# Kernel tuning notes

Hardware: AMD Instinct MI355X
Metric: run time of the kernel (lower is better)

Reference implementation:

```python
import jax, jax.numpy as jnp
import numpy as np

NUM_HEADS = 16
ROPE_BASE = 10000.0


def _rope_cos_sin(seq_len, head_dim, dtype):
    inv_freq = 1.0 / (ROPE_BASE ** (jnp.arange(0, head_dim, 2, dtype=jnp.float32) / head_dim))
    t = jnp.arange(seq_len, dtype=jnp.float32)
    freqs = jnp.einsum('i,j->ij', t, inv_freq)          # [S, hd/2]
    emb = jnp.concatenate([freqs, freqs], axis=-1)      # [S, hd]
    return jnp.cos(emb).astype(dtype), jnp.sin(emb).astype(dtype)


def _rotate_half(x):
    x1, x2 = jnp.split(x, 2, axis=-1)
    return jnp.concatenate([-x2, x1], axis=-1)


def setup_inputs() -> dict:
    key = jax.random.key(0)
    k1, k2, k3 = jax.random.split(key, 3)
    B, S, D = 2, 2048, 2048
    x = jax.random.normal(k1, (B, S, D), dtype=jnp.float32)
    w_qkv = jax.random.normal(k2, (D, 3 * D), dtype=jnp.float32) * (D ** -0.5)
    w_out = jax.random.normal(k3, (D, D), dtype=jnp.float32) * (D ** -0.5)
    return {"x": x, "w_qkv": w_qkv, "w_out": w_out}


def reference(x, w_qkv, w_out):
    B, S, D = x.shape
    H = NUM_HEADS
    hd = D // H
    scale = hd ** -0.5

    qkv = jnp.einsum('bsd,de->bse', x, w_qkv)            # [B,S,3D]
    q, k, v = jnp.split(qkv, 3, axis=-1)
    # -> [B,H,S,hd]
    q = q.reshape(B, S, H, hd).transpose(0, 2, 1, 3)
    k = k.reshape(B, S, H, hd).transpose(0, 2, 1, 3)
    v = v.reshape(B, S, H, hd).transpose(0, 2, 1, 3)

    cos, sin = _rope_cos_sin(S, hd, x.dtype)             # [S,hd]
    cos = cos[None, None]                                # [1,1,S,hd]
    sin = sin[None, None]
    q = q * cos + _rotate_half(q) * sin
    k = k * cos + _rotate_half(k) * sin

    scores = jnp.einsum('bhqd,bhkd->bhqk', q, k) * scale  # [B,H,S,S]
    attn = jax.nn.softmax(scores, axis=-1)                # non-causal: no mask
    out = jnp.einsum('bhqk,bhkd->bhqd', attn, v)          # [B,H,S,hd]
    out = out.transpose(0, 2, 1, 3).reshape(B, S, D)
    out = jnp.einsum('bsd,de->bse', out, w_out)
    return out
```

## Files before the change

kernel.cpp:

```cpp
#include <hip/hip_runtime.h>
#include <hip/hip_bf16.h>

typedef __hip_bfloat16 bf16_t;
typedef __bf16 bf16x8 __attribute__((ext_vector_type(8)));
typedef float floatx4 __attribute__((ext_vector_type(4)));

#define DEVINL __device__ __forceinline__

DEVINL floatx4 mfma16(bf16x8 a, bf16x8 b, floatx4 c) {
  return __builtin_amdgcn_mfma_f32_16x16x32_bf16(a, b, c, 0, 0, 0);
}

DEVINL void gload_lds16(const bf16_t* gp, bf16_t* lp) {
  __builtin_amdgcn_global_load_lds(
      (const __attribute__((address_space(1))) unsigned int*)gp,
      (__attribute__((address_space(3))) unsigned int*)lp, 16, 0, 0);
}

template <class CT> DEVINL CT cvtC(float f);
template <> DEVINL bf16_t cvtC<bf16_t>(float f) { return __float2bfloat16(f); }
template <> DEVINL float cvtC<float>(float f) { return f; }

DEVINL unsigned int pack_bf2(float a, float b) {
  union { bf16_t h; unsigned short s; } ua, ub;
  ua.h = __float2bfloat16(a);
  ub.h = __float2bfloat16(b);
  return (unsigned int)ua.s | ((unsigned int)ub.s << 16);
}

__global__ void convert_f32_bf16(const float* __restrict__ in,
                                 bf16_t* __restrict__ out) {
  size_t i = ((size_t)blockIdx.x * 256 + threadIdx.x) * 8;
  floatx4 a = *(const floatx4*)(in + i);
  floatx4 b = *(const floatx4*)(in + i + 4);
  bf16x8 r;
#pragma unroll
  for (int j = 0; j < 4; j++) r[j] = (__bf16)a[j];
#pragma unroll
  for (int j = 0; j < 4; j++) r[4 + j] = (__bf16)b[j];
  *(bf16x8*)(out + i) = r;
}

template <bool SPLITV, class CT>
__global__ __launch_bounds__(512, 2) void gemm128(
    const bf16_t* __restrict__ A, const bf16_t* __restrict__ BT,
    CT* __restrict__ C, bf16_t* __restrict__ VTout, int M, int N, int CN,
    int K) {
  extern __shared__ __align__(16) char smem[];
  bf16_t* a_lds = (bf16_t*)smem;
  bf16_t* b_lds = a_lds + 24576;

  const int tid = threadIdx.x;
  const int w = tid >> 6;
  const int lane = tid & 63;
  const int quad = lane >> 4;
  const int l16 = lane & 15;
  const int wm = w >> 2, wn = w & 3;

  const int cpx = (int)gridDim.x >> 3;
  const int wgid = ((int)blockIdx.x & 7) * cpx + ((int)blockIdx.x >> 3);
  const int nym = M >> 7;
  const int row0 = (wgid % nym) * 128;
  const int col0 = (wgid / nym) * 256;

  floatx4 acc[4][4] = {};
  bf16x8 af[4][2], bfr[2][2];

  const int nfE = (w >> 1) * 4 + (w & 1);
  const bf16_t* agA = A + (size_t)(row0 + w * 16 + l16) * K + quad * 8;
  const bf16_t* agB = BT + (size_t)(col0 + nfE * 16 + l16) * K + quad * 8;

#define STG_A(sb, tt)                                                      \
  {                                                                        \
    _Pragma("unroll") for (int kc = 0; kc < 2; kc++)                       \
        gload_lds16(agA + (tt) * 64 + kc * 32,                             \
                    a_lds + (sb) * 8192 + w * 1024 + kc * 512);            \
  }
#define STG_BE(sb, tt)                                                     \
  {                                                                        \
    _Pragma("unroll") for (int kc = 0; kc < 2; kc++)                       \
        gload_lds16(agB + (tt) * 64 + kc * 32,                             \
                    b_lds + (sb) * 16384 + nfE * 1024 + kc * 512);         \
  }
#define STG_BO(sb, tt)                                                     \
  {                                                                        \
    _Pragma("unroll") for (int kc = 0; kc < 2; kc++)                       \
        gload_lds16(agB + (size_t)32 * K + (tt) * 64 + kc * 32,            \
                    b_lds + (sb) * 16384 + (nfE + 2) * 1024 + kc * 512);   \
  }
#define LDA(cb)                                                            \
  {                                                                        \
    _Pragma("unroll") for (int m = 0; m < 4; m++)                          \
        _Pragma("unroll") for (int kc = 0; kc < 2; kc++)                   \
            af[m][kc] = *(const bf16x8*)(a_lds + (cb) * 8192 +             \
                                         (wm * 4 + m) * 1024 + kc * 512 +  \
                                         lane * 8);                        \
  }
#define LDB(cb, h)                                                         \
  {                                                                        \
    _Pragma("unroll") for (int jj = 0; jj < 2; jj++)                       \
        _Pragma("unroll") for (int kc = 0; kc < 2; kc++)                   \
            bfr[jj][kc] = *(const bf16x8*)(b_lds + (cb) * 16384 +          \
                                           (wn * 4 + 2 * (h) + jj) * 1024 + \
                                           kc * 512 + lane * 8);           \
  }
#define MM(h)                                                              \
  {                                                                        \
    __builtin_amdgcn_s_setprio(1);                                         \
    _Pragma("unroll") for (int kc = 0; kc < 2; kc++)                       \
        _Pragma("unroll") for (int m = 0; m < 4; m++)                      \
            _Pragma("unroll") for (int jj = 0; jj < 2; jj++)               \
                acc[m][2 * (h) + jj] = mfma16(af[m][kc], bfr[jj][kc],      \
                                              acc[m][2 * (h) + jj]);       \
    __builtin_amdgcn_s_setprio(0);                                         \
  }
#define BAR() __builtin_amdgcn_s_barrier();
#define VM(n) asm volatile("s_waitcnt vmcnt(" #n ")" ::: "memory");
#define LGK() asm volatile("s_waitcnt lgkmcnt(0)" ::: "memory");

#define TILE(tt, cb, sb, DOSTG, V0m, V1m)                  \
  {                                                        \
     LDA(cb); LDB(cb, 0);                            \
    if (DOSTG) { STG_A(sb, (tt) + 2); STG_BE(sb, (tt) + 2); } \
    V0m BAR(); LGK(); MM(0); BAR();                        \
     LDB(cb, 1);                                     \
    if (DOSTG) { STG_BO(sb, (tt) + 2); }                   \
    V1m BAR(); LGK(); MM(1); BAR();                        \
  }

  STG_A(0, 0); STG_BE(0, 0); STG_BO(0, 0);
  STG_A(1, 1); STG_BE(1, 1); STG_BO(1, 1);
  VM(8);
  __builtin_amdgcn_s_barrier();

  const int nt = K >> 6;
  for (int t = 0; t < nt - 2; t += 3) {
    TILE(t, 0, 2, 1, VM(10);, VM(8);)
    TILE(t + 1, 1, 0, 1, VM(10);, VM(8);)
    TILE(t + 2, 2, 1, 1, VM(10);, VM(8);)
  }
  TILE(nt - 2, 0, 0, 0, VM(6);, VM(2);)
  TILE(nt - 1, 1, 0, 0, VM(0);, )

#undef TILE
#undef LGK
#undef VM
#undef BAR
#undef MM
#undef LDB
#undef LDA
#undef STG_BO
#undef STG_BE
#undef STG_A

  if (!SPLITV || col0 < 4096) {
#pragma unroll
    for (int m = 0; m < 4; m++)
#pragma unroll
      for (int n = 0; n < 4; n++)
#pragma unroll
        for (int r = 0; r < 4; r++) {
          int row = row0 + wm * 64 + m * 16 + quad * 4 + r;
          int col = col0 + wn * 64 + n * 16 + l16;
          C[(size_t)row * CN + col] = cvtC<CT>(acc[m][n][r]);
        }
  } else {
    const int b = row0 >> 11;
    const int s0 = row0 & 2047;
    const int h = ((col0 - 4096) >> 7) + (wn >> 1);
    bf16_t* vt = VTout + (size_t)(b * 16 + h) * 128 * 2048;
    struct __align__(8) bf4 { bf16_t v[4]; };
#pragma unroll
    for (int m = 0; m < 4; m++)
#pragma unroll
      for (int n = 0; n < 4; n++) {
        int d = (wn & 1) * 64 + n * 16 + l16;
        int s = s0 + wm * 64 + m * 16 + quad * 4;
        bf4 o;
#pragma unroll
        for (int r = 0; r < 4; r++) o.v[r] = __float2bfloat16(acc[m][n][r]);
        *(bf4*)(vt + (size_t)d * 2048 + s) = o;
      }
  }
}

__global__ void transposecvt(const float* __restrict__ in,
                             bf16_t* __restrict__ out, int M, int N) {
  __shared__ bf16_t tile[32][33];
  int n0 = blockIdx.x * 32, m0 = blockIdx.y * 32;
  tile[threadIdx.y][threadIdx.x] =
      __float2bfloat16(in[(size_t)(m0 + threadIdx.y) * N + n0 + threadIdx.x]);
  __syncthreads();
  out[(size_t)(n0 + threadIdx.y) * M + m0 + threadIdx.x] =
      tile[threadIdx.x][threadIdx.y];
}

__global__ void rope_qk(bf16_t* __restrict__ qkv) {
  struct __align__(8) bf4 { bf16_t v[4]; };
  int t = blockIdx.x * 256 + threadIdx.x;
  int dc = t & 15;
  int s = (t >> 4) & 2047;
  int h = (t >> 15) & 15;
  int b = t >> 19;
  int d = dc * 4;
  size_t base = ((size_t)(b * 2048 + s) * 2) * 2048 + h * 128;
  bf4 ql = *(const bf4*)(qkv + base + d);
  bf4 qh = *(const bf4*)(qkv + base + d + 64);
  bf4 kl = *(const bf4*)(qkv + base + 2048 + d);
  bf4 kh = *(const bf4*)(qkv + base + 2048 + d + 64);
  bf4 oql, oqh, okl, okh;
  const float scale = 0.08838834764831845f;
#pragma unroll
  for (int i = 0; i < 4; i++) {
    int j = d + i;
    float fr = (float)s * exp2f((float)j * -0.20762050593045858f);
    float c, sn;
    __sincosf(fr, &sn, &c);
    float qlo = __bfloat162float(ql.v[i]), qhi = __bfloat162float(qh.v[i]);
    float klo = __bfloat162float(kl.v[i]), khi = __bfloat162float(kh.v[i]);
    oql.v[i] = __float2bfloat16((qlo * c - qhi * sn) * scale);
    oqh.v[i] = __float2bfloat16((qhi * c + qlo * sn) * scale);
    okl.v[i] = __float2bfloat16(klo * c - khi * sn);
    okh.v[i] = __float2bfloat16(khi * c + klo * sn);
  }
  *(bf4*)(qkv + base + d) = oql;
  *(bf4*)(qkv + base + d + 64) = oqh;
  *(bf4*)(qkv + base + 2048 + d) = okl;
  *(bf4*)(qkv + base + 2048 + d + 64) = okh;
}

__global__ __launch_bounds__(256, 2) void flash_attn(
    const bf16_t* __restrict__ qkv, const bf16_t* __restrict__ VT,
    bf16_t* __restrict__ Out) {
  const int S = 2048;
  const int RS = 4096;
  const int tid = threadIdx.x;
  const int wave = tid >> 6;
  const int lane = tid & 63;
  const int quad = lane >> 4;
  const int l16 = lane & 15;

  const int bh = blockIdx.y;
  const int q0 = blockIdx.x * 128;
  const int b = bh >> 4, h = bh & 15;

  const bf16_t* Qb = qkv + (size_t)b * S * RS + h * 128;
  const bf16_t* Kb = Qb + 2048;
  const bf16_t* Vb = VT + (size_t)bh * 128 * S;

  __shared__ __align__(16) bf16_t k_lds[16384];
  __shared__ __align__(16) bf16_t v_lds[16384];

  bf16x8 qf[2][4];
#pragma unroll
  for (int qn = 0; qn < 2; qn++)
#pragma unroll
    for (int ks = 0; ks < 4; ks++)
      qf[qn][ks] = *(const bf16x8*)(
          Qb + (size_t)(q0 + wave * 32 + qn * 16 + l16) * RS + ks * 32 +
          quad * 8);

  floatx4 o_acc[2][8] = {};
  float l_part[2] = {0.f, 0.f};

  const int sA = l16 + 32 * (quad & 1);
  const int sB = sA + 16;
  const bool hi = quad >= 2;

  for (int kt = 0; kt < S / 128; kt++) {
    const int kk0 = kt * 128;
#pragma unroll
    for (int t = 0; t < 2; t++) {
      int mt = wave * 2 + t;
#pragma unroll
      for (int ks = 0; ks < 4; ks++) {
        gload_lds16(Kb + (size_t)(kk0 + mt * 16 + l16) * RS + ks * 32 + quad * 8,
                    k_lds + mt * 2048 + ks * 512);
        gload_lds16(Vb + (size_t)(mt * 16 + l16) * S + kk0 + ks * 32 + quad * 8,
                    v_lds + mt * 2048 + ks * 512);
      }
    }
    __syncthreads();

    floatx4 s_acc[2][8] = {};
    __builtin_amdgcn_s_setprio(1);
#pragma unroll
    for (int ks = 0; ks < 4; ks++)
#pragma unroll
      for (int mt = 0; mt < 8; mt++) {
        bf16x8 kf = *(const bf16x8*)(k_lds + mt * 2048 + ks * 512 + lane * 8);
        s_acc[0][mt] = mfma16(kf, qf[0][ks], s_acc[0][mt]);
        s_acc[1][mt] = mfma16(kf, qf[1][ks], s_acc[1][mt]);
      }
    __builtin_amdgcn_s_setprio(0);

    unsigned int p01[2][8], p23[2][8];
#pragma unroll
    for (int qn = 0; qn < 2; qn++)
#pragma unroll
      for (int mt = 0; mt < 8; mt++) {
        float e0 = __expf(s_acc[qn][mt][0]);
        float e1 = __expf(s_acc[qn][mt][1]);
        float e2 = __expf(s_acc[qn][mt][2]);
        float e3 = __expf(s_acc[qn][mt][3]);
        l_part[qn] += (e0 + e1) + (e2 + e3);
        p01[qn][mt] = pack_bf2(e0, e1);
        p23[qn][mt] = pack_bf2(e2, e3);
      }

#pragma unroll
    for (int kc = 0; kc < 4; kc++) {
      bf16x8 vf[8];
#pragma unroll
      for (int dt = 0; dt < 8; dt++)
        vf[dt] = *(const bf16x8*)(v_lds + dt * 2048 + kc * 512 + lane * 8);
#pragma unroll
      for (int qn = 0; qn < 2; qn++) {
        unsigned int a0 = __shfl(p01[qn][2 * kc], sA);
        unsigned int b0 = __shfl(p01[qn][2 * kc + 1], sA);
        unsigned int a1 = __shfl(p23[qn][2 * kc], sA);
        unsigned int b1 = __shfl(p23[qn][2 * kc + 1], sA);
        unsigned int a2 = __shfl(p01[qn][2 * kc], sB);
        unsigned int b2 = __shfl(p01[qn][2 * kc + 1], sB);
        unsigned int a3 = __shfl(p23[qn][2 * kc], sB);
        unsigned int b3 = __shfl(p23[qn][2 * kc + 1], sB);
        union { unsigned int u[4]; bf16x8 v; } bp;
        bp.u[0] = hi ? b0 : a0;
        bp.u[1] = hi ? b1 : a1;
        bp.u[2] = hi ? b2 : a2;
        bp.u[3] = hi ? b3 : a3;
        __builtin_amdgcn_s_setprio(1);
#pragma unroll
        for (int dt = 0; dt < 8; dt++)
          o_acc[qn][dt] = mfma16(vf[dt], bp.v, o_acc[qn][dt]);
        __builtin_amdgcn_s_setprio(0);
      }
    }
    __syncthreads();
  }

#pragma unroll
  for (int qn = 0; qn < 2; qn++) {
    l_part[qn] += __shfl_xor(l_part[qn], 16);
    l_part[qn] += __shfl_xor(l_part[qn], 32);
  }

  struct __align__(8) bf4 { bf16_t v[4]; };
#pragma unroll
  for (int qn = 0; qn < 2; qn++) {
    float inv = 1.f / l_part[qn];
    size_t s = q0 + wave * 32 + qn * 16 + l16;
#pragma unroll
    for (int dt = 0; dt < 8; dt++) {
      bf4 o;
#pragma unroll
      for (int r = 0; r < 4; r++)
        o.v[r] = __float2bfloat16(o_acc[qn][dt][r] * inv);
      *(bf4*)(Out + ((size_t)b * S + s) * 2048 + h * 128 + dt * 16 + quad * 4) = o;
    }
  }
}

extern "C" void kernel_launch(void* const* d_in, const int* in_sizes, int n_in,
                              void* d_out, int out_size, void* d_ws,
                              size_t ws_size, hipStream_t stream) {
  const float* x = (const float*)d_in[0];
  const float* w_qkv = (const float*)d_in[1];
  const float* w_out = (const float*)d_in[2];
  float* out = (float*)d_out;
  char* ws = (char*)d_ws;

  const int B = 2, S = 2048, D = 2048;
  bf16_t* qkv2 = (bf16_t*)(ws);
  bf16_t* wqkvT = (bf16_t*)(ws + (size_t)B * S * 2 * D * 2);
  bf16_t* xbf = (bf16_t*)(ws + (size_t)B * S * 2 * D * 2 + (size_t)3 * D * D * 2);
  bf16_t* VT = (bf16_t*)(ws + (size_t)B * S * 2 * D * 2 + (size_t)3 * D * D * 2 +
                         (size_t)B * S * D * 2);
  bf16_t* attn = wqkvT;
  bf16_t* woutT = qkv2;

  hipFuncSetAttribute(reinterpret_cast<const void*>(&gemm128<true, bf16_t>),
                      hipFuncAttributeMaxDynamicSharedMemorySize, 147456);
  hipFuncSetAttribute(reinterpret_cast<const void*>(&gemm128<false, float>),
                      hipFuncAttributeMaxDynamicSharedMemorySize, 147456);

  dim3 b32(32, 32);
  convert_f32_bf16<<<(B * S * D) / 2048, 256, 0, stream>>>(x, xbf);
  transposecvt<<<dim3(3 * D / 32, D / 32), b32, 0, stream>>>(w_qkv, wqkvT, D, 3 * D);
  gemm128<true, bf16_t><<<(B * S / 128) * (3 * D / 256), 512, 147456, stream>>>(
      xbf, wqkvT, qkv2, VT, B * S, 3 * D, 2 * D, D);
  rope_qk<<<4096, 256, 0, stream>>>(qkv2);
  flash_attn<<<dim3(S / 128, B * 16), 256, 0, stream>>>(qkv2, VT, attn);
  transposecvt<<<dim3(D / 32, D / 32), b32, 0, stream>>>(w_out, woutT, D, D);
  gemm128<false, float><<<(B * S / 128) * (D / 256), 512, 147456, stream>>>(
      attn, woutT, out, nullptr, B * S, D, D, D);
}
```

Measured before the change: 448.4 us.

## Add 256x256-tile QKV GEMM with quadrant-ping-pong LDS pipeline

```diff
diff --git a/kernel.cpp b/kernel.cpp
--- a/kernel.cpp
+++ b/kernel.cpp
@@ -39,6 +39,162 @@
 #pragma unroll
   for (int j = 0; j < 4; j++) r[4 + j] = (__bf16)b[j];
   *(bf16x8*)(out + i) = r;
+}
+
+template <bool SPLITV, class CT>
+__global__ __launch_bounds__(512, 2) void gemm256(
+    const bf16_t* __restrict__ A, const bf16_t* __restrict__ BT,
+    CT* __restrict__ C, bf16_t* __restrict__ VTout, int M, int N, int CN,
+    int K) {
+  extern __shared__ __align__(16) char smem[];
+  bf16_t* a_lds = (bf16_t*)smem;
+  bf16_t* b_lds = a_lds + 32768;
+
+  const int tid = threadIdx.x;
+  const int w = tid >> 6;
+  const int lane = tid & 63;
+  const int quad = lane >> 4;
+  const int l16 = lane & 15;
+  const int wm = w >> 2, wn = w & 3;
+
+  const int cpx = (int)gridDim.x >> 3;
+  const int wgid = ((int)blockIdx.x & 7) * cpx + ((int)blockIdx.x >> 3);
+  const int nym = M >> 8;
+  const int row0 = (wgid % nym) * 256;
+  const int col0 = (wgid / nym) * 256;
+
+  floatx4 acc[2][2][4][2] = {};
+  bf16x8 af[4][2], bfr[2][2];
+
+  const bf16_t* agA = A + (size_t)(row0 + w * 16 + l16) * K + quad * 8;
+  const bf16_t* agB = BT + (size_t)(col0 + w * 16 + l16) * K + quad * 8;
+  const size_t rK = (size_t)128 * K;
+
+#define STG_A(bb, rp, tt)                                                  \
+  {                                                                        \
+    _Pragma("unroll") for (int kc = 0; kc < 2; kc++)                       \
+        gload_lds16(agA + (rp) * rK + (tt) * 64 + kc * 32,                 \
+                    a_lds + (bb) * 16384 + ((rp) * 8 + w) * 1024 + kc * 512); \
+  }
+#define STG_B(bb, cp, tt)                                                  \
+  {                                                                        \
+    _Pragma("unroll") for (int kc = 0; kc < 2; kc++)                       \
+        gload_lds16(agB + (cp) * rK + (tt) * 64 + kc * 32,                 \
+                    b_lds + (bb) * 16384 + ((cp) * 8 + w) * 1024 + kc * 512); \
+  }
+#define LDA(cb, rp)                                                        \
+  {                                                                        \
+    _Pragma("unroll") for (int m = 0; m < 4; m++)                          \
+        _Pragma("unroll") for (int kc = 0; kc < 2; kc++)                   \
+            af[m][kc] = *(const bf16x8*)(a_lds + (cb) * 16384 +            \
+                                         ((rp) * 8 + wm * 4 + m) * 1024 +  \
+                                         kc * 512 + lane * 8);             \
+  }
+#define LDB(cb, cp)                                                        \
+  {                                                                        \
+    _Pragma("unroll") for (int n = 0; n < 2; n++)                          \
+        _Pragma("unroll") for (int kc = 0; kc < 2; kc++)                   \
+            bfr[n][kc] = *(const bf16x8*)(b_lds + (cb) * 16384 +           \
+                                          ((cp) * 8 + wn * 2 + n) * 1024 + \
+                                          kc * 512 + lane * 8);            \
+  }
+#define MM(rp, cp)                                                         \
+  {                                                                        \
+    __builtin_amdgcn_s_setprio(1);                                         \
+    _Pragma("unroll") for (int kc = 0; kc < 2; kc++)                       \
+        _Pragma("unroll") for (int m = 0; m < 4; m++)                      \
+            _Pragma("unroll") for (int n = 0; n < 2; n++)                  \
+                acc[rp][cp][m][n] =                                        \
+                    mfma16(af[m][kc], bfr[n][kc], acc[rp][cp][m][n]);      \
+    __builtin_amdgcn_s_setprio(0);                                         \
+  }
+#define BAR()                         \
+  {                                   \
+    __builtin_amdgcn_s_barrier();     \
+    __builtin_amdgcn_sched_barrier(0); \
+  }
+#define VM(n)                                              \
+  {                                                        \
+    asm volatile("s_waitcnt vmcnt(" #n ")" ::: "memory");  \
+    __builtin_amdgcn_sched_barrier(0);                     \
+  }
+
+#define TILE(tt, cb, nb, DOSTG, V0m, V1m, V3m)             \
+  {                                                        \
+     LDA(cb, 0); LDB(cb, 0);                         \
+    if (DOSTG) { STG_A(nb, 0, (tt) + 1); STG_B(nb, 0, (tt) + 1); } \
+    V0m BAR(); MM(0, 0); BAR();                            \
+     LDB(cb, 1);                                     \
+    if (DOSTG) STG_B(nb, 1, (tt) + 1);                     \
+    V1m BAR(); MM(0, 1); BAR();                            \
+     LDA(cb, 1);                                     \
+    if (DOSTG) STG_A(nb, 1, (tt) + 1);                     \
+    BAR(); MM(1, 1); BAR();                                \
+     LDB(cb, 0);                                     \
+    V3m BAR(); MM(1, 0); BAR();                            \
+  }
+
+  STG_A(0, 0, 0); STG_B(0, 0, 0); STG_B(0, 1, 0); STG_A(0, 1, 0);
+  VM(4);
+  __builtin_amdgcn_s_barrier();
+  __builtin_amdgcn_sched_barrier(0);
+
+  const int nt = K >> 6;
+  for (int t = 0; t < nt - 2; t += 2) {
+    TILE(t, 0, 1, 1, VM(6);, VM(6);, VM(4);)
+    TILE(t + 1, 1, 0, 1, VM(6);, VM(6);, VM(4);)
+  }
+  TILE(nt - 2, 0, 1, 1, VM(6);, VM(6);, VM(4);)
+  TILE(nt - 1, 1, 0, 0, VM(2);, VM(0);, )
+
+#undef TILE
+#undef VM
+#undef BAR
+#undef MM
+#undef LDB
+#undef LDA
+#undef STG_B
+#undef STG_A
+
+  if (!SPLITV || col0 < 4096) {
+#pragma unroll
+    for (int rp = 0; rp < 2; rp++)
+#pragma unroll
+      for (int cp = 0; cp < 2; cp++)
+#pragma unroll
+        for (int m = 0; m < 4; m++)
+#pragma unroll
+          for (int n = 0; n < 2; n++)
+#pragma unroll
+            for (int r = 0; r < 4; r++) {
+              int row = row0 + rp * 128 + wm * 64 + m * 16 + quad * 4 + r;
+              int col = col0 + cp * 128 + wn * 32 + n * 16 + l16;
+              C[(size_t)row * CN + col] = cvtC<CT>(acc[rp][cp][m][n][r]);
+            }
+  } else {
+    const int b = row0 >> 11;
+    const int s0 = row0 & 2047;
+    struct __align__(8) bf4 { bf16_t v[4]; };
+#pragma unroll
+    for (int cp = 0; cp < 2; cp++) {
+      const int h = ((col0 - 4096) >> 7) + cp;
+      bf16_t* vt = VTout + (size_t)(b * 16 + h) * 128 * 2048;
+#pragma unroll
+      for (int rp = 0; rp < 2; rp++)
+#pragma unroll
+        for (int m = 0; m < 4; m++)
+#pragma unroll
+          for (int n = 0; n < 2; n++) {
+            int d = wn * 32 + n * 16 + l16;
+            int s = s0 + rp * 128 + wm * 64 + m * 16 + quad * 4;
+            bf4 o;
+#pragma unroll
+            for (int r = 0; r < 4; r++)
+              o.v[r] = __float2bfloat16(acc[rp][cp][m][n][r]);
+            *(bf4*)(vt + (size_t)d * 2048 + s) = o;
+          }
+    }
+  }
 }
 
 template <bool SPLITV, class CT>
@@ -379,15 +535,15 @@
   bf16_t* attn = wqkvT;
   bf16_t* woutT = qkv2;
 
-  hipFuncSetAttribute(reinterpret_cast<const void*>(&gemm128<true, bf16_t>),
-                      hipFuncAttributeMaxDynamicSharedMemorySize, 147456);
+  hipFuncSetAttribute(reinterpret_cast<const void*>(&gemm256<true, bf16_t>),
+                      hipFuncAttributeMaxDynamicSharedMemorySize, 131072);
   hipFuncSetAttribute(reinterpret_cast<const void*>(&gemm128<false, float>),
                       hipFuncAttributeMaxDynamicSharedMemorySize, 147456);
 
   dim3 b32(32, 32);
   convert_f32_bf16<<<(B * S * D) / 2048, 256, 0, stream>>>(x, xbf);
   transposecvt<<<dim3(3 * D / 32, D / 32), b32, 0, stream>>>(w_qkv, wqkvT, D, 3 * D);
-  gemm128<true, bf16_t><<<(B * S / 128) * (3 * D / 256), 512, 147456, stream>>>(
+  gemm256<true, bf16_t><<<(B * S / 256) * (3 * D / 256), 512, 131072, stream>>>(
       xbf, wqkvT, qkv2, VT, B * S, 3 * D, 2 * D, D);
   rope_qk<<<4096, 256, 0, stream>>>(qkv2);
   flash_attn<<<dim3(S / 128, B * 16), 256, 0, stream>>>(qkv2, VT, attn);
```

After: 439.5 us. 1.02x faster.
